# Performance work log

Hardware: AMD Instinct MI355X
Metric: run time of the kernel (lower is better)

The kernel has to match this reference:

```python
import jax, jax.numpy as jnp
import numpy as np

N_E, N_C, H = 100000, 50000, 256
D_E, D_C = 768, 1024
E_EE, E_EC, E_CE = 800000, 400000, 400000
EPS = 1e-12


def setup_inputs() -> dict:
    key = jax.random.key(0)
    ks = jax.random.split(key, 16)
    x_entity = jax.random.normal(ks[0], (N_E, D_E), jnp.float32)
    x_chunk = jax.random.normal(ks[1], (N_C, D_C), jnp.float32)
    # edge[0] = source indices, edge[1] = destination indices
    edge_ee = jnp.stack([jax.random.randint(ks[2], (E_EE,), 0, N_E),
                         jax.random.randint(ks[3], (E_EE,), 0, N_E)])
    edge_ec = jnp.stack([jax.random.randint(ks[4], (E_EC,), 0, N_E),
                         jax.random.randint(ks[5], (E_EC,), 0, N_C)])
    edge_ce = jnp.stack([jax.random.randint(ks[6], (E_CE,), 0, N_C),
                         jax.random.randint(ks[7], (E_CE,), 0, N_E)])
    # per-type projection weights (stored [in, out]; y = x @ W)
    P_e = jax.random.normal(ks[8], (D_E, H), jnp.float32) / np.sqrt(D_E).astype(np.float32)
    P_c = jax.random.normal(ks[9], (D_C, H), jnp.float32) / np.sqrt(D_C).astype(np.float32)
    s = np.float32(1.0 / np.sqrt(H))
    # SAGEConv params stacked over the 3 edge types: 0=e->e, 1=e->c, 2=c->e
    Wl1 = jax.random.normal(ks[10], (3, H, H), jnp.float32) * s
    bl1 = jnp.zeros((3, H), jnp.float32)
    Wr1 = jax.random.normal(ks[11], (3, H, H), jnp.float32) * s
    Wl2 = jax.random.normal(ks[12], (3, H, H), jnp.float32) * s
    bl2 = jnp.zeros((3, H), jnp.float32)
    Wr2 = jax.random.normal(ks[13], (3, H, H), jnp.float32) * s
    return {"x_entity": x_entity, "x_chunk": x_chunk,
            "edge_ee": edge_ee, "edge_ec": edge_ec, "edge_ce": edge_ce,
            "P_e": P_e, "P_c": P_c,
            "Wl1": Wl1, "bl1": bl1, "Wr1": Wr1,
            "Wl2": Wl2, "bl2": bl2, "Wr2": Wr2}


def _sage(x_src, x_dst, edge, Wl, bl, Wr, n_dst):
    # PyG SAGEConv: lin_l(mean of neighbor features) + lin_r(x_dst)
    msg = x_src[edge[0]]                                   # [E, H] gather
    agg = jax.ops.segment_sum(msg, edge[1], num_segments=n_dst)
    cnt = jax.ops.segment_sum(jnp.ones((edge.shape[1], 1), x_src.dtype),
                              edge[1], num_segments=n_dst)
    mean = agg / jnp.maximum(cnt, 1.0)                     # isolated nodes -> 0
    return mean @ Wl + bl + x_dst @ Wr


def _l2norm(v):
    # F.normalize(v, dim=1), eps=1e-12
    n = jnp.sqrt(jnp.sum(v * v, axis=1, keepdims=True))
    return v / jnp.maximum(n, EPS)


def reference(x_entity, x_chunk, edge_ee, edge_ec, edge_ce,
              P_e, P_c, Wl1, bl1, Wr1, Wl2, bl2, Wr2):
    # per-type projection (bias=False)
    h_e = x_entity @ P_e
    h_c = x_chunk @ P_c
    id_e, id_c = h_e, h_c
    # conv1: HeteroConv(aggr='sum') -> sum SAGE outputs per destination type
    o_e = (_sage(h_e, h_e, edge_ee, Wl1[0], bl1[0], Wr1[0], N_E)
           + _sage(h_c, h_e, edge_ce, Wl1[2], bl1[2], Wr1[2], N_E))
    o_c = _sage(h_e, h_c, edge_ec, Wl1[1], bl1[1], Wr1[1], N_C)
    # dropout(0.1) is identity in eval; relu then residual
    h_e = jax.nn.relu(o_e) + id_e
    h_c = jax.nn.relu(o_c) + id_c
    # conv2
    o_e = (_sage(h_e, h_e, edge_ee, Wl2[0], bl2[0], Wr2[0], N_E)
           + _sage(h_c, h_e, edge_ce, Wl2[2], bl2[2], Wr2[2], N_E))
    o_c = _sage(h_e, h_c, edge_ec, Wl2[1], bl2[1], Wr2[1], N_C)
    return _l2norm(o_e), _l2norm(o_c)
```

## Files before the change

### kernel.cpp

```cpp
#include <hip/hip_runtime.h>
#include <hip/hip_bf16.h>

#define N_E 100000
#define N_C 50000
#define H 256
#define D_E 768
#define D_C 1024
#define E_EE 800000
#define E_EC 400000
#define E_CE 400000
#define E_TOT (E_EE + E_CE + E_EC)

#define ME_PAD 100096
#define MC_PAD 50048

typedef unsigned short u16;
typedef __attribute__((ext_vector_type(8))) short bf16x8;
typedef __attribute__((ext_vector_type(4))) float f32x4;

__device__ __forceinline__ float bf2f(u16 x) {
    unsigned u = ((unsigned)x) << 16;
    return __builtin_bit_cast(float, u);
}
__device__ __forceinline__ u16 f2bf(float f) {
    unsigned u = __builtin_bit_cast(unsigned, f);
    u = (u + 0x7fffu + ((u >> 16) & 1u)) >> 16;
    return (u16)u;
}

struct TransJobs {
    const float* a[12];
    const float* b[12];
    u16* dst[12];
    int K[12];
};

__global__ __launch_bounds__(1024) void transpose_all_k(TransJobs t) {
    int j = blockIdx.z;
    int K = t.K[j];
    int k0 = blockIdx.x * 32;
    if (k0 >= K) return;
    int n0 = blockIdx.y * 32;
    __shared__ float sm[32][33];
    int tx = threadIdx.x, ty = threadIdx.y;
    size_t idx = (size_t)(k0 + ty) * H + n0 + tx;
    float v = t.a[j][idx];
    if (t.b[j]) v += t.b[j][idx];
    sm[ty][tx] = v;
    __syncthreads();
    t.dst[j][(size_t)(n0 + ty) * K + k0 + tx] = f2bf(sm[tx][ty]);
}

__global__ __launch_bounds__(256) void hist3_k(const int* __restrict__ eeD,
                                               const int* __restrict__ ceD,
                                               const int* __restrict__ ecD,
                                               int* __restrict__ cnt) {
    int i = blockIdx.x * 256 + threadIdx.x;
    if (i >= E_TOT) return;
    if (i < E_EE) atomicAdd(&cnt[eeD[i]], 1);
    else if (i < E_EE + E_CE) atomicAdd(&cnt[N_E + ceD[i - E_EE]], 1);
    else atomicAdd(&cnt[2 * N_E + ecD[i - E_EE - E_CE]], 1);
}

#define SCAN_N (2 * N_E + N_C)
#define SCAN_NB ((SCAN_N + 1023) / 1024)

__global__ __launch_bounds__(1024) void scan_blk_k(const int* __restrict__ cnt,
                                                   int* __restrict__ part,
                                                   int* __restrict__ bsum) {
    __shared__ int sm[1024];
    int i = blockIdx.x * 1024 + threadIdx.x;
    int v = (i < SCAN_N) ? cnt[i] : 0;
    sm[threadIdx.x] = v;
    __syncthreads();
    for (int off = 1; off < 1024; off <<= 1) {
        int t = (threadIdx.x >= off) ? sm[threadIdx.x - off] : 0;
        __syncthreads();
        sm[threadIdx.x] += t;
        __syncthreads();
    }
    if (i < SCAN_N) part[i] = sm[threadIdx.x] - v;
    if (threadIdx.x == 1023) bsum[blockIdx.x] = sm[1023];
}

__global__ __launch_bounds__(1024) void scan_top_k(int* __restrict__ bsum) {
    __shared__ int sm[1024];
    int v = (threadIdx.x < SCAN_NB) ? bsum[threadIdx.x] : 0;
    sm[threadIdx.x] = v;
    __syncthreads();
    for (int off = 1; off < 1024; off <<= 1) {
        int t = (threadIdx.x >= off) ? sm[threadIdx.x - off] : 0;
        __syncthreads();
        sm[threadIdx.x] += t;
        __syncthreads();
    }
    if (threadIdx.x < SCAN_NB) bsum[threadIdx.x] = sm[threadIdx.x] - v;
}

__global__ __launch_bounds__(1024) void scan_out_k(const int* __restrict__ part,
                                                   const int* __restrict__ bsum,
                                                   int* __restrict__ eePtr,
                                                   int* __restrict__ cePtr,
                                                   int* __restrict__ ecPtr,
                                                   int* __restrict__ curAll) {
    int i = blockIdx.x * 1024 + threadIdx.x;
    if (i < SCAN_N) {
        int v = part[i] + bsum[blockIdx.x];
        int w;
        if (i < N_E) {
            w = v; eePtr[i] = w;
        } else if (i < 2 * N_E) {
            w = v - E_EE; cePtr[i - N_E] = w;
        } else {
            w = v - (E_EE + E_CE); ecPtr[i - 2 * N_E] = w;
        }
        curAll[i] = w;
    }
    if (i == 0) {
        eePtr[N_E] = E_EE;
        cePtr[N_E] = E_CE;
        ecPtr[N_C] = E_EC;
    }
}

__global__ __launch_bounds__(256) void reorder3_k(const int* __restrict__ eeS, const int* __restrict__ eeD,
                                                  const int* __restrict__ ceS, const int* __restrict__ ceD,
                                                  const int* __restrict__ ecS, const int* __restrict__ ecD,
                                                  int* __restrict__ curAll, int* __restrict__ srcAll) {
    int i = blockIdx.x * 256 + threadIdx.x;
    if (i >= E_TOT) return;
    if (i < E_EE) {
        int pos = atomicAdd(&curAll[eeD[i]], 1);
        srcAll[pos] = eeS[i];
    } else if (i < E_EE + E_CE) {
        int k = i - E_EE;
        int pos = atomicAdd(&curAll[N_E + ceD[k]], 1);
        srcAll[E_EE + pos] = ceS[k];
    } else {
        int k = i - E_EE - E_CE;
        int pos = atomicAdd(&curAll[2 * N_E + ecD[k]], 1);
        srcAll[E_EE + E_CE + pos] = ecS[k];
    }
}

struct GatherArgs {
    const u16* feat[3];
    const int* rowptr[3];
    const int* srcIdx[3];
    u16* outAgg[3];
    int nDst[3];
    int blkEnd[3];
};

__device__ __forceinline__ void acc8(float* a, uint4 v) {
    a[0] += __builtin_bit_cast(float, v.x << 16);
    a[1] += __builtin_bit_cast(float, v.x & 0xffff0000u);
    a[2] += __builtin_bit_cast(float, v.y << 16);
    a[3] += __builtin_bit_cast(float, v.y & 0xffff0000u);
    a[4] += __builtin_bit_cast(float, v.z << 16);
    a[5] += __builtin_bit_cast(float, v.z & 0xffff0000u);
    a[6] += __builtin_bit_cast(float, v.w << 16);
    a[7] += __builtin_bit_cast(float, v.w & 0xffff0000u);
}

__global__ __launch_bounds__(256) void gather3_k(GatherArgs a) {
    const int b = blockIdx.x;
    const int j = (b >= a.blkEnd[0]) + (b >= a.blkEnd[1]);
    const int b0 = j ? a.blkEnd[j - 1] : 0;
    const int r = (b - b0) * 4 + (threadIdx.x >> 6);
    const int lane = threadIdx.x & 63;
    const int half = lane >> 5;
    const int pos = lane & 31;

    float acc[8] = {};
    int deg = 0;
    if (r < a.nDst[j]) {
        const int* __restrict__ rp = a.rowptr[j];
        const int* __restrict__ si = a.srcIdx[j];
        const u16* __restrict__ ft = a.feat[j];
        int e0 = rp[r], e1 = rp[r + 1];
        deg = e1 - e0;
        int e = e0;
        for (; e + 3 < e1; e += 4) {
            int sA = si[e + half];
            int sB = si[e + 2 + half];
            uint4 vA = *(const uint4*)(ft + (size_t)sA * H + pos * 8);
            uint4 vB = *(const uint4*)(ft + (size_t)sB * H + pos * 8);
            acc8(acc, vA);
            acc8(acc, vB);
        }
        for (; e + 1 < e1; e += 2) {
            int s = si[e + half];
            uint4 v = *(const uint4*)(ft + (size_t)s * H + pos * 8);
            acc8(acc, v);
        }
        if (e < e1 && half == 0) {
            int s = si[e];
            uint4 v = *(const uint4*)(ft + (size_t)s * H + pos * 8);
            acc8(acc, v);
        }
    }
#pragma unroll
    for (int k = 0; k < 8; ++k) acc[k] += __shfl_xor(acc[k], 32);

    if (half == 0) {
        float inv = deg > 0 ? 1.f / (float)deg : 0.f;
        uint4 o;
        o.x = (unsigned)f2bf(acc[0] * inv) | ((unsigned)f2bf(acc[1] * inv) << 16);
        o.y = (unsigned)f2bf(acc[2] * inv) | ((unsigned)f2bf(acc[3] * inv) << 16);
        o.z = (unsigned)f2bf(acc[4] * inv) | ((unsigned)f2bf(acc[5] * inv) << 16);
        o.w = (unsigned)f2bf(acc[6] * inv) | ((unsigned)f2bf(acc[7] * inv) << 16);
        *(uint4*)(a.outAgg[j] + (size_t)r * H + pos * 8) = o;
    }
}

struct GemmCfg {
    const u16* A[3];
    const u16* Wt[3];
    int nPairs;
    const float* bias1;
    const float* bias2;
    const u16* res;
    void* out;
    int Mvalid;
    int mode;
};
struct ConvArgs2 {
    GemmCfg c[2];
    int blkSplit;
};

__global__ __launch_bounds__(512, 4) void gemm_conv_k(ConvArgs2 gg) {
    const int which = blockIdx.x >= gg.blkSplit;
    const GemmCfg* __restrict__ g = which ? &gg.c[1] : &gg.c[0];
    const int row0 = (blockIdx.x - (which ? gg.blkSplit : 0)) * 128;

    __shared__ char lds[2][24576];
    __shared__ float rowsq[128];
    const int tid = threadIdx.x;
    const int lane = tid & 63;
    const int wid = tid >> 6;
    const int wm = wid >> 2;
    const int wn = wid & 3;

    const int srow = tid >> 2;
    const int au = (tid & 3) ^ ((srow >> 1) & 3);
    const int ofsA = (row0 + srow) * H + au * 8;
    const int ofsB1 = srow * H + au * 8;
    const int brow2 = 128 + srow;
    const int bu2 = (tid & 3) ^ ((brow2 >> 1) & 3);
    const int ofsB2 = brow2 * H + bu2 * 8;

    int a_off[4], b_off[4];
#pragma unroll
    for (int mi = 0; mi < 4; ++mi) {
        int row = wm * 64 + mi * 16 + (lane & 15);
        int u = (lane >> 4) ^ ((row >> 1) & 3);
        a_off[mi] = row * 64 + u * 16;
    }
#pragma unroll
    for (int ni = 0; ni < 4; ++ni) {
        int row = wn * 64 + ni * 16 + (lane & 15);
        int u = (lane >> 4) ^ ((row >> 1) & 3);
        b_off[ni] = 8192 + row * 64 + u * 16;
    }

#define STAGE(p_, kk_, ph_)                                                                       \
    do {                                                                                          \
        const u16* A_ = g->A[p_];                                                                 \
        const u16* W_ = g->Wt[p_];                                                                \
        __builtin_amdgcn_global_load_lds(                                                         \
            (const __attribute__((address_space(1))) void*)(A_ + ofsA + (kk_)),                   \
            (__attribute__((address_space(3))) void*)(lds[ph_] + wid * 1024), 16, 0, 0);          \
        __builtin_amdgcn_global_load_lds(                                                         \
            (const __attribute__((address_space(1))) void*)(W_ + ofsB1 + (kk_)),                  \
            (__attribute__((address_space(3))) void*)(lds[ph_] + 8192 + wid * 1024), 16, 0, 0);   \
        __builtin_amdgcn_global_load_lds(                                                         \
            (const __attribute__((address_space(1))) void*)(W_ + ofsB2 + (kk_)),                  \
            (__attribute__((address_space(3))) void*)(lds[ph_] + 16384 + wid * 1024), 16, 0, 0);  \
    } while (0)

    f32x4 acc[4][4] = {};
    const int T = g->nPairs * (H >> 5);

    STAGE(0, 0, 0);
    int pn = 0, kn = 32;
    if (kn == H) { kn = 0; pn = 1; }

    for (int s = 0; s < T; ++s) {
        const int ph = s & 1;
        if (s + 1 < T) {
            STAGE(pn, kn, ph ^ 1);
            kn += 32;
            if (kn == H) { kn = 0; ++pn; }
            asm volatile("s_waitcnt vmcnt(3)" ::: "memory");
        } else {
            asm volatile("s_waitcnt vmcnt(0)" ::: "memory");
        }
        __builtin_amdgcn_sched_barrier(0);
        __builtin_amdgcn_s_barrier();

        bf16x8 af[4], bfr[4];
#pragma unroll
        for (int mi = 0; mi < 4; ++mi)
            af[mi] = *reinterpret_cast<const bf16x8*>(lds[ph] + a_off[mi]);
#pragma unroll
        for (int ni = 0; ni < 4; ++ni)
            bfr[ni] = *reinterpret_cast<const bf16x8*>(lds[ph] + b_off[ni]);
#pragma unroll
        for (int mi = 0; mi < 4; ++mi)
#pragma unroll
            for (int ni = 0; ni < 4; ++ni)
                acc[mi][ni] = __builtin_amdgcn_mfma_f32_16x16x32_bf16(af[mi], bfr[ni],
                                                                      acc[mi][ni], 0, 0, 0);
        __builtin_amdgcn_sched_barrier(0);
        __builtin_amdgcn_s_barrier();
    }
#undef STAGE

    const int ccol = wn * 64 + (lane & 15);
    const int crow0 = row0 + wm * 64 + ((lane >> 4) << 2);
    float bv[4];
#pragma unroll
    for (int ni = 0; ni < 4; ++ni) {
        int c = ccol + ni * 16;
        float b = 0.f;
        if (g->bias1) b += g->bias1[c];
        if (g->bias2) b += g->bias2[c];
        bv[ni] = b;
    }

    if (g->mode == 1) {
#pragma unroll
        for (int ni = 0; ni < 4; ++ni) {
            int c = ccol + ni * 16;
#pragma unroll
            for (int mi = 0; mi < 4; ++mi) {
#pragma unroll
                for (int j = 0; j < 4; ++j) {
                    int r = crow0 + mi * 16 + j;
                    size_t idx = (size_t)r * H + c;
                    float v = fmaxf(acc[mi][ni][j] + bv[ni], 0.f) + bf2f(g->res[idx]);
                    ((u16*)g->out)[idx] = f2bf(v);
                }
            }
        }
    } else {
        if (tid < 128) rowsq[tid] = 0.f;
        __syncthreads();
#pragma unroll
        for (int mi = 0; mi < 4; ++mi) {
#pragma unroll
            for (int j = 0; j < 4; ++j) {
                float p = 0.f;
#pragma unroll
                for (int ni = 0; ni < 4; ++ni) {
                    float v = acc[mi][ni][j] + bv[ni];
                    p += v * v;
                }
                p += __shfl_xor(p, 1);
                p += __shfl_xor(p, 2);
                p += __shfl_xor(p, 4);
                p += __shfl_xor(p, 8);
                if ((lane & 15) == 0) {
                    int rl = wm * 64 + mi * 16 + ((lane >> 4) << 2) + j;
                    atomicAdd(&rowsq[rl], p);
                }
            }
        }
        __syncthreads();
#pragma unroll
        for (int mi = 0; mi < 4; ++mi) {
#pragma unroll
            for (int j = 0; j < 4; ++j) {
                int rl = wm * 64 + mi * 16 + ((lane >> 4) << 2) + j;
                int r = row0 + rl;
                if (r < g->Mvalid) {
                    float inv = 1.f / fmaxf(sqrtf(rowsq[rl]), 1e-12f);
#pragma unroll
                    for (int ni = 0; ni < 4; ++ni) {
                        int c = ccol + ni * 16;
                        float v = acc[mi][ni][j] + bv[ni];
                        ((float*)g->out)[(size_t)r * H + c] = v * inv;
                    }
                }
            }
        }
    }
}

struct ProjArgs2 {
    const float* A[2];
    const u16* Wt[2];
    int K[2];
    int M[2];
    u16* out[2];
    int blkSplit;
};

__global__ __launch_bounds__(512, 4) void gemm_proj_k(ProjArgs2 gg) {
    const int which = blockIdx.x >= gg.blkSplit;
    const int row0 = (blockIdx.x - (which ? gg.blkSplit : 0)) * 128;
    const float* __restrict__ Aptr = gg.A[which];
    const u16* __restrict__ Wt = gg.Wt[which];
    const int K = gg.K[which];
    const int M = gg.M[which];
    u16* __restrict__ outp = gg.out[which];

    __shared__ char lds[2][24576];
    const int tid = threadIdx.x;
    const int lane = tid & 63;
    const int wid = tid >> 6;
    const int wm = wid >> 2;
    const int wn = wid & 3;

    const int srow = tid >> 2;
    const int cunit = tid & 3;
    const int aRow = min(row0 + srow, M - 1);
    const float* pA = Aptr + (size_t)aRow * K + cunit * 8;
    const int aDst = srow * 64 + (cunit ^ ((srow >> 1) & 3)) * 16;

    const int bu1 = cunit ^ ((srow >> 1) & 3);
    const int ofsB1 = srow * K + bu1 * 8;
    const int brow2 = 128 + srow;
    const int bu2 = cunit ^ ((brow2 >> 1) & 3);
    const int ofsB2 = brow2 * K + bu2 * 8;

    int a_off[4], b_off[4];
#pragma unroll
    for (int mi = 0; mi < 4; ++mi) {
        int row = wm * 64 + mi * 16 + (lane & 15);
        int u = (lane >> 4) ^ ((row >> 1) & 3);
        a_off[mi] = row * 64 + u * 16;
    }
#pragma unroll
    for (int ni = 0; ni < 4; ++ni) {
        int row = wn * 64 + ni * 16 + (lane & 15);
        int u = (lane >> 4) ^ ((row >> 1) & 3);
        b_off[ni] = 8192 + row * 64 + u * 16;
    }

#define BSTAGE(kk_, ph_)                                                                          \
    do {                                                                                          \
        __builtin_amdgcn_global_load_lds(                                                         \
            (const __attribute__((address_space(1))) void*)(Wt + ofsB1 + (kk_)),                  \
            (__attribute__((address_space(3))) void*)(lds[ph_] + 8192 + wid * 1024), 16, 0, 0);   \
        __builtin_amdgcn_global_load_lds(                                                         \
            (const __attribute__((address_space(1))) void*)(Wt + ofsB2 + (kk_)),                  \
            (__attribute__((address_space(3))) void*)(lds[ph_] + 16384 + wid * 1024), 16, 0, 0);  \
    } while (0)

    f32x4 acc[4][4] = {};
    const int T = K >> 5;

    BSTAGE(0, 0);
    float4 c0 = *reinterpret_cast<const float4*>(pA);
    float4 c1 = *reinterpret_cast<const float4*>(pA + 4);

    for (int s = 0; s < T; ++s) {
        const int ph = s & 1;
        float4 n0 = make_float4(0.f, 0.f, 0.f, 0.f), n1 = n0;
        if (s + 1 < T) {
            BSTAGE((s + 1) * 32, ph ^ 1);
            n0 = *reinterpret_cast<const float4*>(pA + (s + 1) * 32);
            n1 = *reinterpret_cast<const float4*>(pA + (s + 1) * 32 + 4);
        }
        union { bf16x8 v; u16 e[8]; } pk;
        pk.e[0] = f2bf(c0.x); pk.e[1] = f2bf(c0.y); pk.e[2] = f2bf(c0.z); pk.e[3] = f2bf(c0.w);
        pk.e[4] = f2bf(c1.x); pk.e[5] = f2bf(c1.y); pk.e[6] = f2bf(c1.z); pk.e[7] = f2bf(c1.w);
        *reinterpret_cast<bf16x8*>(lds[ph] + aDst) = pk.v;
        asm volatile("s_waitcnt lgkmcnt(0)" ::: "memory");
        __builtin_amdgcn_sched_barrier(0);
        __builtin_amdgcn_s_barrier();

        bf16x8 af[4], bfr[4];
#pragma unroll
        for (int mi = 0; mi < 4; ++mi)
            af[mi] = *reinterpret_cast<const bf16x8*>(lds[ph] + a_off[mi]);
#pragma unroll
        for (int ni = 0; ni < 4; ++ni)
            bfr[ni] = *reinterpret_cast<const bf16x8*>(lds[ph] + b_off[ni]);
#pragma unroll
        for (int mi = 0; mi < 4; ++mi)
#pragma unroll
            for (int ni = 0; ni < 4; ++ni)
                acc[mi][ni] = __builtin_amdgcn_mfma_f32_16x16x32_bf16(af[mi], bfr[ni],
                                                                      acc[mi][ni], 0, 0, 0);
        __builtin_amdgcn_sched_barrier(0);
        __builtin_amdgcn_s_barrier();
        c0 = n0; c1 = n1;
    }
#undef BSTAGE

    const int ccol = wn * 64 + (lane & 15);
    const int crow0 = row0 + wm * 64 + ((lane >> 4) << 2);
#pragma unroll
    for (int ni = 0; ni < 4; ++ni) {
        int c = ccol + ni * 16;
#pragma unroll
        for (int mi = 0; mi < 4; ++mi) {
#pragma unroll
            for (int j = 0; j < 4; ++j) {
                int r = crow0 + mi * 16 + j;
                outp[(size_t)r * H + c] = f2bf(acc[mi][ni][j]);
            }
        }
    }
}

extern "C" void kernel_launch(void* const* d_in, const int* in_sizes, int n_in,
                              void* d_out, int out_size, void* d_ws, size_t ws_size,
                              hipStream_t stream) {
    const float* x_e = (const float*)d_in[0];
    const float* x_c = (const float*)d_in[1];
    const int* e_ee = (const int*)d_in[2];
    const int* e_ec = (const int*)d_in[3];
    const int* e_ce = (const int*)d_in[4];
    const float* P_e = (const float*)d_in[5];
    const float* P_c = (const float*)d_in[6];
    const float* Wl1 = (const float*)d_in[7];
    const float* bl1 = (const float*)d_in[8];
    const float* Wr1 = (const float*)d_in[9];
    const float* Wl2 = (const float*)d_in[10];
    const float* bl2 = (const float*)d_in[11];
    const float* Wr2 = (const float*)d_in[12];
    float* out = (float*)d_out;

    const size_t EHp = (size_t)ME_PAD * H;
    const size_t CHp = (size_t)MC_PAD * H;

    u16* us = (u16*)d_ws;
    u16* he0 = us;   us += EHp;
    u16* he1 = us;   us += EHp;
    u16* aggE1 = us; us += EHp;
    u16* aggE2 = us; us += EHp;
    u16* hc0 = us;   us += CHp;
    u16* hc1 = us;   us += CHp;
    u16* aggC = us;  us += CHp;
    u16* PeT = us;   us += H * D_E;
    u16* PcT = us;   us += H * D_C;
    u16* WlT1 = us;  us += 3 * H * H;
    u16* WrT1_1 = us; us += H * H;
    u16* WrT1s = us;  us += H * H;
    u16* WlT2 = us;  us += 3 * H * H;
    u16* WrT2_1 = us; us += H * H;
    u16* WrT2s = us;  us += H * H;

    int* ip = (int*)us;
    int* eePtr = ip;  ip += N_E + 1;
    int* cePtr = ip;  ip += N_E + 1;
    int* ecPtr = ip;  ip += N_C + 1;
    int* curAll = ip; ip += SCAN_N;
    int* srcAll = ip; ip += E_TOT;
    int* cntAll = ip; ip += SCAN_N;
    int* part = ip;   ip += SCAN_N;
    int* bsum = ip;   ip += SCAN_NB + 1;

    const int WHH = H * H;

    hipMemsetAsync(cntAll, 0, (size_t)SCAN_N * sizeof(int), stream);
    hist3_k<<<(E_TOT + 255) / 256, 256, 0, stream>>>(e_ee + E_EE, e_ce + E_CE, e_ec + E_EC, cntAll);
    scan_blk_k<<<SCAN_NB, 1024, 0, stream>>>(cntAll, part, bsum);
    scan_top_k<<<1, 1024, 0, stream>>>(bsum);
    scan_out_k<<<SCAN_NB, 1024, 0, stream>>>(part, bsum, eePtr, cePtr, ecPtr, curAll);
    reorder3_k<<<(E_TOT + 255) / 256, 256, 0, stream>>>(e_ee, e_ee + E_EE, e_ce, e_ce + E_CE,
                                                        e_ec, e_ec + E_EC, curAll, srcAll);
    const int* eeSrc = srcAll;
    const int* ceSrc = srcAll + E_EE;
    const int* ecSrc = srcAll + E_EE + E_CE;

    {
        TransJobs t{};
        int n = 0;
        auto add = [&](const float* a, const float* b, u16* d, int K) {
            t.a[n] = a; t.b[n] = b; t.dst[n] = d; t.K[n] = K; ++n;
        };
        add(P_e, nullptr, PeT, D_E);
        add(P_c, nullptr, PcT, D_C);
        for (int p = 0; p < 3; ++p) add(Wl1 + p * WHH, nullptr, WlT1 + p * WHH, H);
        for (int p = 0; p < 3; ++p) add(Wl2 + p * WHH, nullptr, WlT2 + p * WHH, H);
        add(Wr1 + 1 * WHH, nullptr, WrT1_1, H);
        add(Wr2 + 1 * WHH, nullptr, WrT2_1, H);
        add(Wr1 + 0 * WHH, Wr1 + 2 * WHH, WrT1s, H);
        add(Wr2 + 0 * WHH, Wr2 + 2 * WHH, WrT2s, H);
        transpose_all_k<<<dim3(D_C / 32, H / 32, 12), dim3(32, 32), 0, stream>>>(t);
    }

    const int gridE = ME_PAD / 128, gridC = MC_PAD / 128;

    {
        ProjArgs2 g{};
        g.A[0] = x_e; g.Wt[0] = PeT; g.K[0] = D_E; g.M[0] = N_E; g.out[0] = he0;
        g.A[1] = x_c; g.Wt[1] = PcT; g.K[1] = D_C; g.M[1] = N_C; g.out[1] = hc0;
        g.blkSplit = gridE;
        gemm_proj_k<<<gridE + gridC, 512, 0, stream>>>(g);
    }

    const int gBlkE = ME_PAD / 4, gBlkC = MC_PAD / 4;
    const int gTotal = 2 * gBlkE + gBlkC;

    {
        GatherArgs a{};
        a.feat[0] = he0; a.rowptr[0] = eePtr; a.srcIdx[0] = eeSrc; a.outAgg[0] = aggE1; a.nDst[0] = N_E;
        a.feat[1] = hc0; a.rowptr[1] = cePtr; a.srcIdx[1] = ceSrc; a.outAgg[1] = aggE2; a.nDst[1] = N_E;
        a.feat[2] = he0; a.rowptr[2] = ecPtr; a.srcIdx[2] = ecSrc; a.outAgg[2] = aggC;  a.nDst[2] = N_C;
        a.blkEnd[0] = gBlkE; a.blkEnd[1] = 2 * gBlkE; a.blkEnd[2] = gTotal;
        gather3_k<<<gTotal, 256, 0, stream>>>(a);
    }
    {
        ConvArgs2 g{};
        g.c[0].A[0] = aggE1; g.c[0].Wt[0] = WlT1 + 0 * WHH;
        g.c[0].A[1] = aggE2; g.c[0].Wt[1] = WlT1 + 2 * WHH;
        g.c[0].A[2] = he0;   g.c[0].Wt[2] = WrT1s;
        g.c[0].nPairs = 3;
        g.c[0].bias1 = bl1 + 0 * H; g.c[0].bias2 = bl1 + 2 * H;
        g.c[0].res = he0; g.c[0].out = he1; g.c[0].mode = 1;
        g.c[1].A[0] = aggC; g.c[1].Wt[0] = WlT1 + 1 * WHH;
        g.c[1].A[1] = hc0;  g.c[1].Wt[1] = WrT1_1;
        g.c[1].nPairs = 2;
        g.c[1].bias1 = bl1 + 1 * H;
        g.c[1].res = hc0; g.c[1].out = hc1; g.c[1].mode = 1;
        g.blkSplit = gridE;
        gemm_conv_k<<<gridE + gridC, 512, 0, stream>>>(g);
    }

    {
        GatherArgs a{};
        a.feat[0] = he1; a.rowptr[0] = eePtr; a.srcIdx[0] = eeSrc; a.outAgg[0] = aggE1; a.nDst[0] = N_E;
        a.feat[1] = hc1; a.rowptr[1] = cePtr; a.srcIdx[1] = ceSrc; a.outAgg[1] = aggE2; a.nDst[1] = N_E;
        a.feat[2] = he1; a.rowptr[2] = ecPtr; a.srcIdx[2] = ecSrc; a.outAgg[2] = aggC;  a.nDst[2] = N_C;
        a.blkEnd[0] = gBlkE; a.blkEnd[1] = 2 * gBlkE; a.blkEnd[2] = gTotal;
        gather3_k<<<gTotal, 256, 0, stream>>>(a);
    }
    {
        ConvArgs2 g{};
        g.c[0].A[0] = aggE1; g.c[0].Wt[0] = WlT2 + 0 * WHH;
        g.c[0].A[1] = aggE2; g.c[0].Wt[1] = WlT2 + 2 * WHH;
        g.c[0].A[2] = he1;   g.c[0].Wt[2] = WrT2s;
        g.c[0].nPairs = 3;
        g.c[0].bias1 = bl2 + 0 * H; g.c[0].bias2 = bl2 + 2 * H;
        g.c[0].out = out; g.c[0].Mvalid = N_E; g.c[0].mode = 2;
        g.c[1].A[0] = aggC; g.c[1].Wt[0] = WlT2 + 1 * WHH;
        g.c[1].A[1] = hc1;  g.c[1].Wt[1] = WrT2_1;
        g.c[1].nPairs = 2;
        g.c[1].bias1 = bl2 + 1 * H;
        g.c[1].out = out + (size_t)N_E * H; g.c[1].Mvalid = N_C; g.c[1].mode = 2;
        g.blkSplit = gridE;
        gemm_conv_k<<<gridE + gridC, 512, 0, stream>>>(g);
    }
}
```

Before: 893.4 us.

## Triple-buffer LDS in conv and projection GEMMs; unroll gather loop by eight

Both GEMM kernels move from a double-buffered to a triple-buffered LDS pipeline, prefetching two K-steps ahead with matching vmcnt waits and rotating buffer pointers. The projection kernel also keeps two register sets of fp32 A prefetches and unrolls the loop by two. The gather kernel gets an 8-edge unrolled loop so more independent row loads are in flight. The aim is to hide global memory latency better. The cost is 50% more LDS per block, which may lower occupancy against the 4-blocks launch bound, plus higher register pressure.

```diff
diff --git a/kernel.cpp b/kernel.cpp
--- a/kernel.cpp
+++ b/kernel.cpp
@@ -13,6 +13,8 @@
 
 #define ME_PAD 100096
 #define MC_PAD 50048
+
+#define LDSZ 24576
 
 typedef unsigned short u16;
 typedef __attribute__((ext_vector_type(8))) short bf16x8;
@@ -181,13 +183,23 @@
         int e0 = rp[r], e1 = rp[r + 1];
         deg = e1 - e0;
         int e = e0;
+        for (; e + 7 < e1; e += 8) {
+            int sA = si[e + half];
+            int sB = si[e + 2 + half];
+            int sC = si[e + 4 + half];
+            int sD = si[e + 6 + half];
+            uint4 vA = *(const uint4*)(ft + (size_t)sA * H + pos * 8);
+            uint4 vB = *(const uint4*)(ft + (size_t)sB * H + pos * 8);
+            uint4 vC = *(const uint4*)(ft + (size_t)sC * H + pos * 8);
+            uint4 vD = *(const uint4*)(ft + (size_t)sD * H + pos * 8);
+            acc8(acc, vA); acc8(acc, vB); acc8(acc, vC); acc8(acc, vD);
+        }
         for (; e + 3 < e1; e += 4) {
             int sA = si[e + half];
             int sB = si[e + 2 + half];
             uint4 vA = *(const uint4*)(ft + (size_t)sA * H + pos * 8);
             uint4 vB = *(const uint4*)(ft + (size_t)sB * H + pos * 8);
-            acc8(acc, vA);
-            acc8(acc, vB);
+            acc8(acc, vA); acc8(acc, vB);
         }
         for (; e + 1 < e1; e += 2) {
             int s = si[e + half];
@@ -235,7 +247,7 @@
     const GemmCfg* __restrict__ g = which ? &gg.c[1] : &gg.c[0];
     const int row0 = (blockIdx.x - (which ? gg.blkSplit : 0)) * 128;
 
-    __shared__ char lds[2][24576];
+    __shared__ char lds[3][LDSZ];
     __shared__ float rowsq[128];
     const int tid = threadIdx.x;
     const int lane = tid & 63;
@@ -265,34 +277,40 @@
         b_off[ni] = 8192 + row * 64 + u * 16;
     }
 
-#define STAGE(p_, kk_, ph_)                                                                       \
+#define STAGE(p_, kk_, buf_)                                                                      \
     do {                                                                                          \
         const u16* A_ = g->A[p_];                                                                 \
         const u16* W_ = g->Wt[p_];                                                                \
         __builtin_amdgcn_global_load_lds(                                                         \
             (const __attribute__((address_space(1))) void*)(A_ + ofsA + (kk_)),                   \
-            (__attribute__((address_space(3))) void*)(lds[ph_] + wid * 1024), 16, 0, 0);          \
+            (__attribute__((address_space(3))) void*)((buf_) + wid * 1024), 16, 0, 0);            \
         __builtin_amdgcn_global_load_lds(                                                         \
             (const __attribute__((address_space(1))) void*)(W_ + ofsB1 + (kk_)),                  \
-            (__attribute__((address_space(3))) void*)(lds[ph_] + 8192 + wid * 1024), 16, 0, 0);   \
+            (__attribute__((address_space(3))) void*)((buf_) + 8192 + wid * 1024), 16, 0, 0);     \
         __builtin_amdgcn_global_load_lds(                                                         \
             (const __attribute__((address_space(1))) void*)(W_ + ofsB2 + (kk_)),                  \
-            (__attribute__((address_space(3))) void*)(lds[ph_] + 16384 + wid * 1024), 16, 0, 0);  \
+            (__attribute__((address_space(3))) void*)((buf_) + 16384 + wid * 1024), 16, 0, 0);    \
     } while (0)
 
     f32x4 acc[4][4] = {};
     const int T = g->nPairs * (H >> 5);
 
-    STAGE(0, 0, 0);
-    int pn = 0, kn = 32;
+    char* bufC = lds[0];
+    char* bufN = lds[1];
+    char* bufS = lds[2];
+
+    STAGE(0, 0, bufC);
+    STAGE(0, 32, bufN);
+    int pn = 0, kn = 64;
     if (kn == H) { kn = 0; pn = 1; }
 
     for (int s = 0; s < T; ++s) {
-        const int ph = s & 1;
-        if (s + 1 < T) {
-            STAGE(pn, kn, ph ^ 1);
+        if (s + 2 < T) {
+            STAGE(pn, kn, bufS);
             kn += 32;
             if (kn == H) { kn = 0; ++pn; }
+            asm volatile("s_waitcnt vmcnt(6)" ::: "memory");
+        } else if (s + 1 < T) {
             asm volatile("s_waitcnt vmcnt(3)" ::: "memory");
         } else {
             asm volatile("s_waitcnt vmcnt(0)" ::: "memory");
@@ -303,10 +321,10 @@
         bf16x8 af[4], bfr[4];
 #pragma unroll
         for (int mi = 0; mi < 4; ++mi)
-            af[mi] = *reinterpret_cast<const bf16x8*>(lds[ph] + a_off[mi]);
+            af[mi] = *reinterpret_cast<const bf16x8*>(bufC + a_off[mi]);
 #pragma unroll
         for (int ni = 0; ni < 4; ++ni)
-            bfr[ni] = *reinterpret_cast<const bf16x8*>(lds[ph] + b_off[ni]);
+            bfr[ni] = *reinterpret_cast<const bf16x8*>(bufC + b_off[ni]);
 #pragma unroll
         for (int mi = 0; mi < 4; ++mi)
 #pragma unroll
@@ -315,6 +333,7 @@
                                                                       acc[mi][ni], 0, 0, 0);
         __builtin_amdgcn_sched_barrier(0);
         __builtin_amdgcn_s_barrier();
+        char* t = bufC; bufC = bufN; bufN = bufS; bufS = t;
     }
 #undef STAGE
 
@@ -407,7 +426,7 @@
     const int M = gg.M[which];
     u16* __restrict__ outp = gg.out[which];
 
-    __shared__ char lds[2][24576];
+    __shared__ char lds[3][LDSZ];
     const int tid = threadIdx.x;
     const int lane = tid & 63;
     const int wid = tid >> 6;
@@ -440,56 +459,77 @@
         b_off[ni] = 8192 + row * 64 + u * 16;
     }
 
-#define BSTAGE(kk_, ph_)                                                                          \
+#define BSTAGE(kk_, buf_)                                                                         \
     do {                                                                                          \
         __builtin_amdgcn_global_load_lds(                                                         \
             (const __attribute__((address_space(1))) void*)(Wt + ofsB1 + (kk_)),                  \
-            (__attribute__((address_space(3))) void*)(lds[ph_] + 8192 + wid * 1024), 16, 0, 0);   \
+            (__attribute__((address_space(3))) void*)((buf_) + 8192 + wid * 1024), 16, 0, 0);     \
         __builtin_amdgcn_global_load_lds(                                                         \
             (const __attribute__((address_space(1))) void*)(Wt + ofsB2 + (kk_)),                  \
-            (__attribute__((address_space(3))) void*)(lds[ph_] + 16384 + wid * 1024), 16, 0, 0);  \
+            (__attribute__((address_space(3))) void*)((buf_) + 16384 + wid * 1024), 16, 0, 0);    \
     } while (0)
 
     f32x4 acc[4][4] = {};
     const int T = K >> 5;
 
-    BSTAGE(0, 0);
-    float4 c0 = *reinterpret_cast<const float4*>(pA);
-    float4 c1 = *reinterpret_cast<const float4*>(pA + 4);
-
-    for (int s = 0; s < T; ++s) {
-        const int ph = s & 1;
-        float4 n0 = make_float4(0.f, 0.f, 0.f, 0.f), n1 = n0;
-        if (s + 1 < T) {
-            BSTAGE((s + 1) * 32, ph ^ 1);
-            n0 = *reinterpret_cast<const float4*>(pA + (s + 1) * 32);
-            n1 = *reinterpret_cast<const float4*>(pA + (s + 1) * 32 + 4);
-        }
-        union { bf16x8 v; u16 e[8]; } pk;
-        pk.e[0] = f2bf(c0.x); pk.e[1] = f2bf(c0.y); pk.e[2] = f2bf(c0.z); pk.e[3] = f2bf(c0.w);
-        pk.e[4] = f2bf(c1.x); pk.e[5] = f2bf(c1.y); pk.e[6] = f2bf(c1.z); pk.e[7] = f2bf(c1.w);
-        *reinterpret_cast<bf16x8*>(lds[ph] + aDst) = pk.v;
-        asm volatile("s_waitcnt lgkmcnt(0)" ::: "memory");
-        __builtin_amdgcn_sched_barrier(0);
-        __builtin_amdgcn_s_barrier();
-
-        bf16x8 af[4], bfr[4];
-#pragma unroll
-        for (int mi = 0; mi < 4; ++mi)
-            af[mi] = *reinterpret_cast<const bf16x8*>(lds[ph] + a_off[mi]);
-#pragma unroll
-        for (int ni = 0; ni < 4; ++ni)
-            bfr[ni] = *reinterpret_cast<const bf16x8*>(lds[ph] + b_off[ni]);
-#pragma unroll
-        for (int mi = 0; mi < 4; ++mi)
-#pragma unroll
-            for (int ni = 0; ni < 4; ++ni)
-                acc[mi][ni] = __builtin_amdgcn_mfma_f32_16x16x32_bf16(af[mi], bfr[ni],
-                                                                      acc[mi][ni], 0, 0, 0);
-        __builtin_amdgcn_sched_barrier(0);
-        __builtin_amdgcn_s_barrier();
-        c0 = n0; c1 = n1;
-    }
+    char* bufC = lds[0];
+    char* bufN = lds[1];
+    char* bufS = lds[2];
+
+    BSTAGE(0, bufC);
+    float4 cA0 = *reinterpret_cast<const float4*>(pA);
+    float4 cA1 = *reinterpret_cast<const float4*>(pA + 4);
+    BSTAGE(32, bufN);
+    float4 cB0 = *reinterpret_cast<const float4*>(pA + 32);
+    float4 cB1 = *reinterpret_cast<const float4*>(pA + 36);
+
+#define PITER(s_, c0_, c1_)                                                                       \
+    do {                                                                                          \
+        const int s = (s_);                                                                       \
+        if (s + 2 < T) {                                                                          \
+            BSTAGE((s + 2) * 32, bufS);                                                           \
+            asm volatile("s_waitcnt vmcnt(6)" ::: "memory");                                      \
+        } else if (s + 1 < T) {                                                                   \
+            asm volatile("s_waitcnt vmcnt(4)" ::: "memory");                                      \
+        } else {                                                                                  \
+            asm volatile("s_waitcnt vmcnt(0)" ::: "memory");                                      \
+        }                                                                                         \
+        union { bf16x8 v; u16 e[8]; } pk;                                                         \
+        pk.e[0] = f2bf(c0_.x); pk.e[1] = f2bf(c0_.y);                                             \
+        pk.e[2] = f2bf(c0_.z); pk.e[3] = f2bf(c0_.w);                                             \
+        pk.e[4] = f2bf(c1_.x); pk.e[5] = f2bf(c1_.y);                                             \
+        pk.e[6] = f2bf(c1_.z); pk.e[7] = f2bf(c1_.w);                                             \
+        *reinterpret_cast<bf16x8*>(bufC + aDst) = pk.v;                                           \
+        if (s + 2 < T) {                                                                          \
+            c0_ = *reinterpret_cast<const float4*>(pA + (s + 2) * 32);                            \
+            c1_ = *reinterpret_cast<const float4*>(pA + (s + 2) * 32 + 4);                        \
+        }                                                                                         \
+        asm volatile("s_waitcnt lgkmcnt(0)" ::: "memory");                                        \
+        __builtin_amdgcn_sched_barrier(0);                                                        \
+        __builtin_amdgcn_s_barrier();                                                             \
+        bf16x8 af[4], bfr[4];                                                                     \
+        _Pragma("unroll")                                                                         \
+        for (int mi = 0; mi < 4; ++mi)                                                            \
+            af[mi] = *reinterpret_cast<const bf16x8*>(bufC + a_off[mi]);                          \
+        _Pragma("unroll")                                                                         \
+        for (int ni = 0; ni < 4; ++ni)                                                            \
+            bfr[ni] = *reinterpret_cast<const bf16x8*>(bufC + b_off[ni]);                         \
+        _Pragma("unroll")                                                                         \
+        for (int mi = 0; mi < 4; ++mi)                                                            \
+            _Pragma("unroll")                                                                     \
+            for (int ni = 0; ni < 4; ++ni)                                                        \
+                acc[mi][ni] = __builtin_amdgcn_mfma_f32_16x16x32_bf16(af[mi], bfr[ni],            \
+                                                                      acc[mi][ni], 0, 0, 0);      \
+        __builtin_amdgcn_sched_barrier(0);                                                        \
+        __builtin_amdgcn_s_barrier();                                                             \
+        char* t_ = bufC; bufC = bufN; bufN = bufS; bufS = t_;                                     \
+    } while (0)
+
+    for (int s2 = 0; s2 < T; s2 += 2) {
+        PITER(s2, cA0, cA1);
+        PITER(s2 + 1, cB0, cB1);
+    }
+#undef PITER
 #undef BSTAGE
 
     const int ccol = wn * 64 + (lane & 15);
```

Result: faster. 869.0 us (-2.7%).

## Triple-buffer GEMM LDS stages, drop trailing barrier, add setprio, unroll gather by 8

Applied to the files above, without the earlier changes.

Both GEMM kernels move from double to triple LDS buffering with rotating buffer pointers. This lets the second s_barrier per k-step be removed, since the buffer being refilled is no longer the one just read. The MFMA section is wrapped in s_setprio, and the projection kernel now waits explicitly on vmcnt before the barrier. The gather kernel gets an 8-edge unrolled loop to keep more loads in flight. The larger LDS footprint (72KB per block) may lower occupancy relative to launch_bounds(512,4), and dropping the barrier depends on the three-buffer spacing being enough for correctness.

```diff
diff --git a/kernel.cpp b/kernel.cpp
--- a/kernel.cpp
+++ b/kernel.cpp
@@ -13,6 +13,8 @@
 
 #define ME_PAD 100096
 #define MC_PAD 50048
+
+#define LDSZ 24576
 
 typedef unsigned short u16;
 typedef __attribute__((ext_vector_type(8))) short bf16x8;
@@ -181,13 +183,23 @@
         int e0 = rp[r], e1 = rp[r + 1];
         deg = e1 - e0;
         int e = e0;
+        for (; e + 7 < e1; e += 8) {
+            int sA = si[e + half];
+            int sB = si[e + 2 + half];
+            int sC = si[e + 4 + half];
+            int sD = si[e + 6 + half];
+            uint4 vA = *(const uint4*)(ft + (size_t)sA * H + pos * 8);
+            uint4 vB = *(const uint4*)(ft + (size_t)sB * H + pos * 8);
+            uint4 vC = *(const uint4*)(ft + (size_t)sC * H + pos * 8);
+            uint4 vD = *(const uint4*)(ft + (size_t)sD * H + pos * 8);
+            acc8(acc, vA); acc8(acc, vB); acc8(acc, vC); acc8(acc, vD);
+        }
         for (; e + 3 < e1; e += 4) {
             int sA = si[e + half];
             int sB = si[e + 2 + half];
             uint4 vA = *(const uint4*)(ft + (size_t)sA * H + pos * 8);
             uint4 vB = *(const uint4*)(ft + (size_t)sB * H + pos * 8);
-            acc8(acc, vA);
-            acc8(acc, vB);
+            acc8(acc, vA); acc8(acc, vB);
         }
         for (; e + 1 < e1; e += 2) {
             int s = si[e + half];
@@ -235,7 +247,7 @@
     const GemmCfg* __restrict__ g = which ? &gg.c[1] : &gg.c[0];
     const int row0 = (blockIdx.x - (which ? gg.blkSplit : 0)) * 128;
 
-    __shared__ char lds[2][24576];
+    __shared__ char lds[3][LDSZ];
     __shared__ float rowsq[128];
     const int tid = threadIdx.x;
     const int lane = tid & 63;
@@ -265,32 +277,35 @@
         b_off[ni] = 8192 + row * 64 + u * 16;
     }
 
-#define STAGE(p_, kk_, ph_)                                                                       \
+#define STAGE(p_, kk_, buf_)                                                                      \
     do {                                                                                          \
         const u16* A_ = g->A[p_];                                                                 \
         const u16* W_ = g->Wt[p_];                                                                \
         __builtin_amdgcn_global_load_lds(                                                         \
             (const __attribute__((address_space(1))) void*)(A_ + ofsA + (kk_)),                   \
-            (__attribute__((address_space(3))) void*)(lds[ph_] + wid * 1024), 16, 0, 0);          \
+            (__attribute__((address_space(3))) void*)((buf_) + wid * 1024), 16, 0, 0);            \
         __builtin_amdgcn_global_load_lds(                                                         \
             (const __attribute__((address_space(1))) void*)(W_ + ofsB1 + (kk_)),                  \
-            (__attribute__((address_space(3))) void*)(lds[ph_] + 8192 + wid * 1024), 16, 0, 0);   \
+            (__attribute__((address_space(3))) void*)((buf_) + 8192 + wid * 1024), 16, 0, 0);     \
         __builtin_amdgcn_global_load_lds(                                                         \
             (const __attribute__((address_space(1))) void*)(W_ + ofsB2 + (kk_)),                  \
-            (__attribute__((address_space(3))) void*)(lds[ph_] + 16384 + wid * 1024), 16, 0, 0);  \
+            (__attribute__((address_space(3))) void*)((buf_) + 16384 + wid * 1024), 16, 0, 0);    \
     } while (0)
 
     f32x4 acc[4][4] = {};
     const int T = g->nPairs * (H >> 5);
 
-    STAGE(0, 0, 0);
+    char* bufC = lds[0];
+    char* bufN = lds[1];
+    char* bufT = lds[2];
+
+    STAGE(0, 0, bufC);
     int pn = 0, kn = 32;
     if (kn == H) { kn = 0; pn = 1; }
 
     for (int s = 0; s < T; ++s) {
-        const int ph = s & 1;
         if (s + 1 < T) {
-            STAGE(pn, kn, ph ^ 1);
+            STAGE(pn, kn, bufN);
             kn += 32;
             if (kn == H) { kn = 0; ++pn; }
             asm volatile("s_waitcnt vmcnt(3)" ::: "memory");
@@ -300,21 +315,23 @@
         __builtin_amdgcn_sched_barrier(0);
         __builtin_amdgcn_s_barrier();
 
+        __builtin_amdgcn_s_setprio(1);
         bf16x8 af[4], bfr[4];
 #pragma unroll
         for (int mi = 0; mi < 4; ++mi)
-            af[mi] = *reinterpret_cast<const bf16x8*>(lds[ph] + a_off[mi]);
+            af[mi] = *reinterpret_cast<const bf16x8*>(bufC + a_off[mi]);
 #pragma unroll
         for (int ni = 0; ni < 4; ++ni)
-            bfr[ni] = *reinterpret_cast<const bf16x8*>(lds[ph] + b_off[ni]);
+            bfr[ni] = *reinterpret_cast<const bf16x8*>(bufC + b_off[ni]);
 #pragma unroll
         for (int mi = 0; mi < 4; ++mi)
 #pragma unroll
             for (int ni = 0; ni < 4; ++ni)
                 acc[mi][ni] = __builtin_amdgcn_mfma_f32_16x16x32_bf16(af[mi], bfr[ni],
                                                                       acc[mi][ni], 0, 0, 0);
+        __builtin_amdgcn_s_setprio(0);
         __builtin_amdgcn_sched_barrier(0);
-        __builtin_amdgcn_s_barrier();
+        char* t = bufC; bufC = bufN; bufN = bufT; bufT = t;
     }
 #undef STAGE
 
@@ -407,7 +424,7 @@
     const int M = gg.M[which];
     u16* __restrict__ outp = gg.out[which];
 
-    __shared__ char lds[2][24576];
+    __shared__ char lds[3][LDSZ];
     const int tid = threadIdx.x;
     const int lane = tid & 63;
     const int wid = tid >> 6;
@@ -440,55 +457,64 @@
         b_off[ni] = 8192 + row * 64 + u * 16;
     }
 
-#define BSTAGE(kk_, ph_)                                                                          \
+#define BSTAGE(kk_, buf_)                                                                         \
     do {                                                                                          \
         __builtin_amdgcn_global_load_lds(                                                         \
             (const __attribute__((address_space(1))) void*)(Wt + ofsB1 + (kk_)),                  \
-            (__attribute__((address_space(3))) void*)(lds[ph_] + 8192 + wid * 1024), 16, 0, 0);   \
+            (__attribute__((address_space(3))) void*)((buf_) + 8192 + wid * 1024), 16, 0, 0);     \
         __builtin_amdgcn_global_load_lds(                                                         \
             (const __attribute__((address_space(1))) void*)(Wt + ofsB2 + (kk_)),                  \
-            (__attribute__((address_space(3))) void*)(lds[ph_] + 16384 + wid * 1024), 16, 0, 0);  \
+            (__attribute__((address_space(3))) void*)((buf_) + 16384 + wid * 1024), 16, 0, 0);    \
     } while (0)
 
     f32x4 acc[4][4] = {};
     const int T = K >> 5;
 
-    BSTAGE(0, 0);
+    char* bufC = lds[0];
+    char* bufN = lds[1];
+    char* bufT = lds[2];
+
+    BSTAGE(0, bufC);
     float4 c0 = *reinterpret_cast<const float4*>(pA);
     float4 c1 = *reinterpret_cast<const float4*>(pA + 4);
 
     for (int s = 0; s < T; ++s) {
-        const int ph = s & 1;
-        float4 n0 = make_float4(0.f, 0.f, 0.f, 0.f), n1 = n0;
+        float4 n0, n1;
         if (s + 1 < T) {
-            BSTAGE((s + 1) * 32, ph ^ 1);
+            BSTAGE((s + 1) * 32, bufN);
             n0 = *reinterpret_cast<const float4*>(pA + (s + 1) * 32);
             n1 = *reinterpret_cast<const float4*>(pA + (s + 1) * 32 + 4);
+            asm volatile("s_waitcnt vmcnt(4)" ::: "memory");
+        } else {
+            n0 = make_float4(0.f, 0.f, 0.f, 0.f); n1 = n0;
+            asm volatile("s_waitcnt vmcnt(0)" ::: "memory");
         }
         union { bf16x8 v; u16 e[8]; } pk;
         pk.e[0] = f2bf(c0.x); pk.e[1] = f2bf(c0.y); pk.e[2] = f2bf(c0.z); pk.e[3] = f2bf(c0.w);
         pk.e[4] = f2bf(c1.x); pk.e[5] = f2bf(c1.y); pk.e[6] = f2bf(c1.z); pk.e[7] = f2bf(c1.w);
-        *reinterpret_cast<bf16x8*>(lds[ph] + aDst) = pk.v;
+        *reinterpret_cast<bf16x8*>(bufC + aDst) = pk.v;
         asm volatile("s_waitcnt lgkmcnt(0)" ::: "memory");
         __builtin_amdgcn_sched_barrier(0);
         __builtin_amdgcn_s_barrier();
 
+        __builtin_amdgcn_s_setprio(1);
         bf16x8 af[4], bfr[4];
 #pragma unroll
         for (int mi = 0; mi < 4; ++mi)
-            af[mi] = *reinterpret_cast<const bf16x8*>(lds[ph] + a_off[mi]);
+            af[mi] = *reinterpret_cast<const bf16x8*>(bufC + a_off[mi]);
 #pragma unroll
         for (int ni = 0; ni < 4; ++ni)
-            bfr[ni] = *reinterpret_cast<const bf16x8*>(lds[ph] + b_off[ni]);
+            bfr[ni] = *reinterpret_cast<const bf16x8*>(bufC + b_off[ni]);
 #pragma unroll
         for (int mi = 0; mi < 4; ++mi)
 #pragma unroll
             for (int ni = 0; ni < 4; ++ni)
                 acc[mi][ni] = __builtin_amdgcn_mfma_f32_16x16x32_bf16(af[mi], bfr[ni],
                                                                       acc[mi][ni], 0, 0, 0);
+        __builtin_amdgcn_s_setprio(0);
         __builtin_amdgcn_sched_barrier(0);
-        __builtin_amdgcn_s_barrier();
         c0 = n0; c1 = n1;
+        char* t = bufC; bufC = bufN; bufN = bufT; bufT = t;
     }
 #undef BSTAGE
 
```

New measurement: 886.0 us. About the same (-0.8%).
